# Performance work log

Hardware: AMD Instinct MI355X
Metric: run time of the kernel (lower is better)

Reference implementation:

```python
import jax, jax.numpy as jnp
import numpy as np

N = 100000          # number of nodes
E = 128             # embedding size
NUM_LAYERS = 4
SMOOTH = 12.0       # MAXIMUM_SMOOTHNESS
RELATIONS = [("at", 2), ("clear", 1), ("on", 2)]  # sorted, as in module
ATOM_COUNTS = {"at": 150000, "clear": 150000, "on": 150000}


def mish(x):
    return x * jnp.tanh(jax.nn.softplus(x))


def _linear_init(k, din, dout):
    s = 1.0 / np.sqrt(din)
    kw, kb = jax.random.split(k)
    w = jax.random.uniform(kw, (din, dout), jnp.float32, -s, s)
    b = jax.random.uniform(kb, (dout,), jnp.float32, -s, s)
    return w, b


def setup_inputs() -> dict:
    key = jax.random.key(0)
    ks = iter(jax.random.split(key, 64))
    inp = {}
    inp["node_embeddings"] = jax.random.normal(next(ks), (N, E), jnp.float32)
    for name, ar in RELATIONS:
        inp[f"atoms_{name}"] = jax.random.randint(
            next(ks), (ATOM_COUNTS[name] * ar,), 0, N, dtype=jnp.int32)
        d = ar * E
        inp[f"w_in_{name}"], inp[f"b_in_{name}"] = _linear_init(next(ks), d, d)
        inp[f"w_out_{name}"], inp[f"b_out_{name}"] = _linear_init(next(ks), d, d)
    # update MLP: Linear(2E, 2E) -> mish -> Linear(2E, E)
    inp["w_u_in"], inp["b_u_in"] = _linear_init(next(ks), 2 * E, 2 * E)
    inp["w_u_out"], inp["b_u_out"] = _linear_init(next(ks), 2 * E, E)
    return inp


def _forward(node_embeddings, atoms, params):
    w_u_in, b_u_in, w_u_out, b_u_out = params["update"]

    def layer(h):
        msgs, idxs = [], []
        for name, ar in RELATIONS:
            w_in, b_in, w_out, b_out = params[name]
            av = atoms[name]                              # [A*ar] node indices
            x = h[av].reshape(-1, ar * E)                 # gather -> [A, ar*E]
            y = x + (mish(x @ w_in + b_in) @ w_out + b_out)  # residual MLP
            msgs.append(y.reshape(-1, E))
            idxs.append(av)
        msg = jnp.concatenate(msgs, 0)                    # [T, E]
        idx = jnp.concatenate(idxs, 0)                    # [T]
        # smooth-max aggregation (max offsets are not differentiated)
        seg_max = jax.ops.segment_max(msg, idx, num_segments=N)
        seg_max = jnp.where(jnp.isfinite(seg_max), seg_max, 0.0)  # empty -> 0 (include_self=False on zeros)
        seg_max = jax.lax.stop_gradient(seg_max)
        exps = jnp.exp(SMOOTH * (msg - seg_max[idx]))
        exps_sum = jax.ops.segment_sum(exps, idx, num_segments=N) + 1e-16
        max_msg = jnp.log(exps_sum) / SMOOTH + seg_max
        upd_in = jnp.concatenate([max_msg, h], axis=1)    # [N, 2E]
        upd = mish(upd_in @ w_u_in + b_u_in) @ w_u_out + b_u_out
        return h + upd                                    # outer residual

    h = node_embeddings
    for _ in range(NUM_LAYERS):
        h = layer(h)
    return h


def reference(node_embeddings, atoms_at, atoms_clear, atoms_on,
              w_in_at, b_in_at, w_out_at, b_out_at,
              w_in_clear, b_in_clear, w_out_clear, b_out_clear,
              w_in_on, b_in_on, w_out_on, b_out_on,
              w_u_in, b_u_in, w_u_out, b_u_out):
    atoms = {"at": atoms_at, "clear": atoms_clear, "on": atoms_on}
    params = {
        "at": (w_in_at, b_in_at, w_out_at, b_out_at),
        "clear": (w_in_clear, b_in_clear, w_out_clear, b_out_clear),
        "on": (w_in_on, b_in_on, w_out_on, b_out_on),
        "update": (w_u_in, b_u_in, w_u_out, b_u_out),
    }
    return _forward(node_embeddings, atoms, params)
```

## Files before the change

### kernel.cpp

```cpp
#include <hip/hip_runtime.h>
#include <hip/hip_bf16.h>
#include <math.h>

#define NNODES 100000
#define EDIM 128
#define TSLOTS 750000
#define NB 391

typedef __bf16 bf16x8 __attribute__((ext_vector_type(8)));
typedef __bf16 bf16x4 __attribute__((ext_vector_type(4)));
typedef float f32x4 __attribute__((ext_vector_type(4)));

#define T_SCALE 17.312340490667562f
#define INV_SCALE 0.05776226504666211f
#define EMPTY_V (-3.0701134f)

__device__ __forceinline__ float mishf(float x) {
  float u = __expf(fminf(x, 15.f));
  float num = u * (u + 2.f);
  return x * num * __builtin_amdgcn_rcpf(num + 2.f);
}

__device__ __forceinline__ double exp12t(float t) {
  t = fmaxf(t, -20000.f);
  float ti = floorf(t);
  float m = exp2f(t - ti);
  int ei = (int)ti;
  ei = ei < -1000 ? -1000 : (ei > 1000 ? 1000 : ei);
  return (double)m * __longlong_as_double(((long long)(1023 + ei)) << 52);
}

__device__ __forceinline__ float logS12(double S) {
  if (!(S > 0.0)) return EMPTY_V;
  long long b = __double_as_longlong(S);
  int e2 = (int)((b >> 52) & 0x7FF) - 1023;
  float mf = __uint_as_float(0x3F800000u | (unsigned)((b >> 29) & 0x7FFFFF));
  return ((float)e2 + log2f(mf)) * INV_SCALE;
}

__global__ void k_sentinel(float* out, int n) {
  int i = blockIdx.x * 256 + threadIdx.x;
  if (i < n) out[i] = 1.0e6f;
}

__global__ void k_init(const float* __restrict__ h0, __bf16* __restrict__ hb, int n8) {
  int i = blockIdx.x * 256 + threadIdx.x;
  if (i >= n8) return;
  float4 f0 = ((const float4*)h0)[i * 2];
  float4 f1 = ((const float4*)h0)[i * 2 + 1];
  bf16x8 p = {(__bf16)f0.x, (__bf16)f0.y, (__bf16)f0.z, (__bf16)f0.w,
              (__bf16)f1.x, (__bf16)f1.y, (__bf16)f1.z, (__bf16)f1.w};
  *(bf16x8*)(hb + (size_t)i * 8) = p;
}

struct TransDesc {
  const float* src[8];
  __bf16* dst[8];
  int R[8];
  int C[8];
  int tstart[9];
};

__global__ void k_transpose_all(TransDesc td) {
  __shared__ float tile[32][33];
  int b = blockIdx.x;
  int m = 0;
  while (m < 7 && b >= td.tstart[m + 1]) m++;
  int t = b - td.tstart[m];
  int R = td.R[m], C = td.C[m];
  int tcols = C >> 5;
  int by = t / tcols, bx = t - by * tcols;
  int tx = threadIdx.x & 31, ty = threadIdx.x >> 5;
  const float* src = td.src[m];
  __bf16* dst = td.dst[m];
  for (int i = 0; i < 32; i += 8)
    tile[ty + i][tx] = src[(size_t)(by * 32 + ty + i) * C + bx * 32 + tx];
  __syncthreads();
  for (int i = 0; i < 32; i += 8)
    dst[(size_t)(bx * 32 + ty + i) * R + by * 32 + tx] = (__bf16)tile[tx][ty + i];
}

__device__ __forceinline__ int slot_node(int s, const int* at, const int* cl, const int* on) {
  if (s < 300000) return at[s];
  if (s < 450000) return cl[s - 300000];
  return on[s - 450000];
}

__global__ void k_count(const int* __restrict__ at, const int* __restrict__ cl,
                        const int* __restrict__ on, int* __restrict__ cnt) {
  int s = blockIdx.x * 256 + threadIdx.x;
  if (s >= TSLOTS) return;
  atomicAdd(&cnt[slot_node(s, at, cl, on)], 1);
}

__global__ void k_bsum(const int* __restrict__ cnt, int* __restrict__ bsum) {
  __shared__ int sm[256];
  int n = blockIdx.x * 256 + threadIdx.x;
  sm[threadIdx.x] = (n < NNODES) ? cnt[n] : 0;
  __syncthreads();
  for (int st = 128; st > 0; st >>= 1) {
    if (threadIdx.x < st) sm[threadIdx.x] += sm[threadIdx.x + st];
    __syncthreads();
  }
  if (threadIdx.x == 0) bsum[blockIdx.x] = sm[0];
}

__global__ void k_bscan(const int* __restrict__ bsum, int* __restrict__ bpre,
                        int* __restrict__ off) {
  __shared__ int sm[512];
  int t = threadIdx.x;
  int v = (t < NB) ? bsum[t] : 0;
  sm[t] = v;
  __syncthreads();
  for (int st = 1; st < 512; st <<= 1) {
    int x = (t >= st) ? sm[t - st] : 0;
    __syncthreads();
    sm[t] += x;
    __syncthreads();
  }
  if (t < NB) bpre[t] = sm[t] - v;
  if (t == NB - 1) off[NNODES] = sm[t];
}

__global__ void k_off(const int* __restrict__ cnt, const int* __restrict__ bpre,
                      int* __restrict__ off) {
  __shared__ int sm[256];
  int n = blockIdx.x * 256 + threadIdx.x;
  int v = (n < NNODES) ? cnt[n] : 0;
  sm[threadIdx.x] = v;
  __syncthreads();
  for (int st = 1; st < 256; st <<= 1) {
    int t = (threadIdx.x >= st) ? sm[threadIdx.x - st] : 0;
    __syncthreads();
    sm[threadIdx.x] += t;
    __syncthreads();
  }
  if (n < NNODES) off[n] = bpre[blockIdx.x] + sm[threadIdx.x] - v;
}

__global__ void k_fill(const int* __restrict__ at, const int* __restrict__ cl,
                       const int* __restrict__ on, const int* __restrict__ off,
                       int* __restrict__ cnt, int* __restrict__ perm) {
  int s = blockIdx.x * 256 + threadIdx.x;
  if (s >= TSLOTS) return;
  int node = slot_node(s, at, cl, on);
  int pos = atomicAdd(&cnt[node], -1) - 1;
  perm[s] = off[node] + pos;
}

__global__ __launch_bounds__(256, 4) void k_rel2(
    const float* __restrict__ hf, const __bf16* __restrict__ hb,
    const int* __restrict__ av,
    const __bf16* __restrict__ wt1, const float* __restrict__ b1,
    const __bf16* __restrict__ wt2, const float* __restrict__ b2,
    _Float16* __restrict__ msg, const int* __restrict__ permrel, int A) {
  __shared__ __align__(16) __bf16 xs[64][264];
  __shared__ int prm[128];
  const int tid = threadIdx.x;
  const int lane = tid & 63;
  const int w = tid >> 6;
  const int row0 = blockIdx.x * 64;

  if (tid < 128) {
    int i2 = row0 * 2 + tid;
    prm[tid] = (i2 < 2 * A) ? permrel[i2] : 0;
  }
  if (hb != nullptr) {
    for (int i = 0; i < 8; ++i) {
      int s = tid + i * 256;
      int r = s >> 5, o = s & 31;
      int a = row0 + r;
      uint4 v = {0, 0, 0, 0};
      if (a < A) {
        int node = av[2 * a + (o >> 4)];
        v = *(const uint4*)(hb + (size_t)node * 128 + (o & 15) * 8);
      }
      *(uint4*)&xs[r][o * 8] = v;
    }
  } else {
    for (int i = 0; i < 16; ++i) {
      int s = tid + i * 256;
      int r = s >> 6, o = s & 63;
      int a = row0 + r;
      float4 f = {0.f, 0.f, 0.f, 0.f};
      if (a < A) {
        int node = av[2 * a + (o >> 5)];
        f = *(const float4*)(hf + (size_t)node * 128 + (o & 31) * 4);
      }
      bf16x4 p = {(__bf16)f.x, (__bf16)f.y, (__bf16)f.z, (__bf16)f.w};
      *(bf16x4*)&xs[r][o * 4] = p;
    }
  }
  __syncthreads();

  const int lhi = lane >> 4, llo = lane & 15;
  const int cb = w * 64;

  f32x4 acc1[4][4];
#pragma unroll
  for (int rt = 0; rt < 4; rt++)
#pragma unroll
    for (int ct = 0; ct < 4; ct++) acc1[rt][ct] = (f32x4){0.f, 0.f, 0.f, 0.f};

#pragma unroll
  for (int kk = 0; kk < 8; ++kk) {
    int k = kk * 32 + lhi * 8;
    bf16x8 af[4], bfr[4];
#pragma unroll
    for (int rt = 0; rt < 4; rt++) af[rt] = *(const bf16x8*)&xs[rt * 16 + llo][k];
#pragma unroll
    for (int ct = 0; ct < 4; ct++)
      bfr[ct] = *(const bf16x8*)(wt1 + (size_t)(cb + ct * 16 + llo) * 256 + k);
#pragma unroll
    for (int rt = 0; rt < 4; rt++)
#pragma unroll
      for (int ct = 0; ct < 4; ct++)
        acc1[rt][ct] = __builtin_amdgcn_mfma_f32_16x16x32_bf16(af[rt], bfr[ct], acc1[rt][ct], 0, 0, 0);
  }
  __syncthreads();

  float b1v[4];
#pragma unroll
  for (int ct = 0; ct < 4; ct++) b1v[ct] = b1[cb + ct * 16 + llo];
#pragma unroll
  for (int rt = 0; rt < 4; rt++)
#pragma unroll
    for (int ct = 0; ct < 4; ct++)
#pragma unroll
      for (int i = 0; i < 4; i++)
        xs[rt * 16 + lhi * 4 + i][cb + ct * 16 + llo] = (__bf16)mishf(acc1[rt][ct][i] + b1v[ct]);
  __syncthreads();

  f32x4 acc2[4][4];
#pragma unroll
  for (int rt = 0; rt < 4; rt++)
#pragma unroll
    for (int ct = 0; ct < 4; ct++) acc2[rt][ct] = (f32x4){0.f, 0.f, 0.f, 0.f};

#pragma unroll
  for (int kk = 0; kk < 8; ++kk) {
    int k = kk * 32 + lhi * 8;
    bf16x8 af[4], bfr[4];
#pragma unroll
    for (int rt = 0; rt < 4; rt++) af[rt] = *(const bf16x8*)&xs[rt * 16 + llo][k];
#pragma unroll
    for (int ct = 0; ct < 4; ct++)
      bfr[ct] = *(const bf16x8*)(wt2 + (size_t)(cb + ct * 16 + llo) * 256 + k);
#pragma unroll
    for (int rt = 0; rt < 4; rt++)
#pragma unroll
      for (int ct = 0; ct < 4; ct++)
        acc2[rt][ct] = __builtin_amdgcn_mfma_f32_16x16x32_bf16(af[rt], bfr[ct], acc2[rt][ct], 0, 0, 0);
  }
  __syncthreads();

  float b2v[4];
#pragma unroll
  for (int ct = 0; ct < 4; ct++) b2v[ct] = b2[cb + ct * 16 + llo];
  ushort* zs = (ushort*)&xs[0][0];
#pragma unroll
  for (int rt = 0; rt < 4; rt++)
#pragma unroll
    for (int ct = 0; ct < 4; ct++)
#pragma unroll
      for (int i = 0; i < 4; i++) {
        int r = rt * 16 + lhi * 4 + i;
        int col = cb + ct * 16 + llo;
        union { ushort u; _Float16 f; } cv;
        cv.f = (_Float16)(acc2[rt][ct][i] + b2v[ct]);
        zs[r * 264 + col] = cv.u;
      }
  __syncthreads();

  for (int i = 0; i < 8; ++i) {
    int s = tid + i * 256;
    int sr = s >> 4;
    int c = s & 15;
    int a = row0 + (sr >> 1);
    if (a < A) {
      int rr = sr >> 1, c0 = (sr & 1) * 128 + c * 8;
      uint4 z = *(const uint4*)&zs[rr * 264 + c0];
      *(uint4*)(msg + (size_t)prm[sr] * 128 + c * 8) = z;
    }
  }
}

__global__ __launch_bounds__(256, 4) void k_rel1(
    const float* __restrict__ hf, const __bf16* __restrict__ hb,
    const int* __restrict__ av,
    const __bf16* __restrict__ wt1, const float* __restrict__ b1,
    const __bf16* __restrict__ wt2, const float* __restrict__ b2,
    _Float16* __restrict__ msg, const int* __restrict__ permrel, int A) {
  __shared__ __align__(16) __bf16 xs[64][136];
  __shared__ int prm[64];
  const int tid = threadIdx.x;
  const int lane = tid & 63;
  const int w = tid >> 6;
  const int row0 = blockIdx.x * 64;

  if (tid < 64) {
    int a = row0 + tid;
    prm[tid] = (a < A) ? permrel[a] : 0;
  }
  if (hb != nullptr) {
    for (int i = 0; i < 4; ++i) {
      int s = tid + i * 256;
      int r = s >> 4, o = s & 15;
      int a = row0 + r;
      uint4 v = {0, 0, 0, 0};
      if (a < A) {
        int node = av[a];
        v = *(const uint4*)(hb + (size_t)node * 128 + o * 8);
      }
      *(uint4*)&xs[r][o * 8] = v;
    }
  } else {
    for (int i = 0; i < 8; ++i) {
      int s = tid + i * 256;
      int r = s >> 5, o = s & 31;
      int a = row0 + r;
      float4 f = {0.f, 0.f, 0.f, 0.f};
      if (a < A) {
        int node = av[a];
        f = *(const float4*)(hf + (size_t)node * 128 + o * 4);
      }
      bf16x4 p = {(__bf16)f.x, (__bf16)f.y, (__bf16)f.z, (__bf16)f.w};
      *(bf16x4*)&xs[r][o * 4] = p;
    }
  }
  __syncthreads();

  const int lhi = lane >> 4, llo = lane & 15;
  const int cb = w * 32;

  f32x4 acc1[4][2];
#pragma unroll
  for (int rt = 0; rt < 4; rt++)
#pragma unroll
    for (int ct = 0; ct < 2; ct++) acc1[rt][ct] = (f32x4){0.f, 0.f, 0.f, 0.f};

#pragma unroll
  for (int kk = 0; kk < 4; ++kk) {
    int k = kk * 32 + lhi * 8;
    bf16x8 af[4], bfr[2];
#pragma unroll
    for (int rt = 0; rt < 4; rt++) af[rt] = *(const bf16x8*)&xs[rt * 16 + llo][k];
#pragma unroll
    for (int ct = 0; ct < 2; ct++)
      bfr[ct] = *(const bf16x8*)(wt1 + (size_t)(cb + ct * 16 + llo) * 128 + k);
#pragma unroll
    for (int rt = 0; rt < 4; rt++)
#pragma unroll
      for (int ct = 0; ct < 2; ct++)
        acc1[rt][ct] = __builtin_amdgcn_mfma_f32_16x16x32_bf16(af[rt], bfr[ct], acc1[rt][ct], 0, 0, 0);
  }
  __syncthreads();

  float b1v[2];
#pragma unroll
  for (int ct = 0; ct < 2; ct++) b1v[ct] = b1[cb + ct * 16 + llo];
#pragma unroll
  for (int rt = 0; rt < 4; rt++)
#pragma unroll
    for (int ct = 0; ct < 2; ct++)
#pragma unroll
      for (int i = 0; i < 4; i++)
        xs[rt * 16 + lhi * 4 + i][cb + ct * 16 + llo] = (__bf16)mishf(acc1[rt][ct][i] + b1v[ct]);
  __syncthreads();

  f32x4 acc2[4][2];
#pragma unroll
  for (int rt = 0; rt < 4; rt++)
#pragma unroll
    for (int ct = 0; ct < 2; ct++) acc2[rt][ct] = (f32x4){0.f, 0.f, 0.f, 0.f};

#pragma unroll
  for (int kk = 0; kk < 4; ++kk) {
    int k = kk * 32 + lhi * 8;
    bf16x8 af[4], bfr[2];
#pragma unroll
    for (int rt = 0; rt < 4; rt++) af[rt] = *(const bf16x8*)&xs[rt * 16 + llo][k];
#pragma unroll
    for (int ct = 0; ct < 2; ct++)
      bfr[ct] = *(const bf16x8*)(wt2 + (size_t)(cb + ct * 16 + llo) * 128 + k);
#pragma unroll
    for (int rt = 0; rt < 4; rt++)
#pragma unroll
      for (int ct = 0; ct < 2; ct++)
        acc2[rt][ct] = __builtin_amdgcn_mfma_f32_16x16x32_bf16(af[rt], bfr[ct], acc2[rt][ct], 0, 0, 0);
  }
  __syncthreads();

  float b2v[2];
#pragma unroll
  for (int ct = 0; ct < 2; ct++) b2v[ct] = b2[cb + ct * 16 + llo];
  ushort* zs = (ushort*)&xs[0][0];
#pragma unroll
  for (int rt = 0; rt < 4; rt++)
#pragma unroll
    for (int ct = 0; ct < 2; ct++)
#pragma unroll
      for (int i = 0; i < 4; i++) {
        int r = rt * 16 + lhi * 4 + i;
        int col = cb + ct * 16 + llo;
        union { ushort u; _Float16 f; } cv;
        cv.f = (_Float16)(acc2[rt][ct][i] + b2v[ct]);
        zs[r * 136 + col] = cv.u;
      }
  __syncthreads();

  for (int i = 0; i < 4; ++i) {
    int s = tid + i * 256;
    int sr = s >> 4;
    int c = s & 15;
    int a = row0 + sr;
    if (a < A) {
      uint4 z = *(const uint4*)&zs[sr * 136 + c * 8];
      *(uint4*)(msg + (size_t)prm[sr] * 128 + c * 8) = z;
    }
  }
}

__global__ __launch_bounds__(256, 8) void k_agg(
    const _Float16* __restrict__ msg, const int* __restrict__ off,
    const float* __restrict__ hf, const __bf16* __restrict__ hb,
    __bf16* __restrict__ mm) {
  __shared__ int offs[33];
  const int tid = threadIdx.x;
  const int lane = tid & 63;
  const int w = tid >> 6;
  const int node0 = blockIdx.x * 32;
  if (tid < 33) {
    int n = node0 + tid;
    offs[tid] = off[n < NNODES ? n : NNODES];
  }
  __syncthreads();

  const int fl = lane & 31;
  const int p = lane >> 5;
  const _Float16* mb = msg + fl * 4;

#pragma unroll 1
  for (int j = 0; j < 8; ++j) {
    int n = node0 + w * 8 + j;
    if (n >= NNODES) break;
    float h0, h1, h2, h3;
    if (hb != nullptr) {
      bf16x4 hq = *(const bf16x4*)(hb + (size_t)n * 128 + fl * 4);
      h0 = (float)hq[0]; h1 = (float)hq[1]; h2 = (float)hq[2]; h3 = (float)hq[3];
    } else {
      float4 hq = *(const float4*)(hf + (size_t)n * 128 + fl * 4);
      h0 = hq.x; h1 = hq.y; h2 = hq.z; h3 = hq.w;
    }
    int beg = offs[w * 8 + j];
    int deg = offs[w * 8 + j + 1] - beg;
    double S0 = 0.0, S1 = 0.0, S2 = 0.0, S3 = 0.0;
#pragma unroll 1
    for (int d = 0; d < deg; d += 2) {
      int rp = d + p;
      int rc = rp < deg - 1 ? rp : deg - 1;
      uint2 v = *(const uint2*)(mb + (size_t)(beg + rc) * 128);
      if (rp >= deg) { v.x = 0xFC00FC00u; v.y = 0xFC00FC00u; }
      union { uint2 u; _Float16 f[4]; } q;
      q.u = v;
      S0 += exp12t(((float)q.f[0] + h0) * T_SCALE);
      S1 += exp12t(((float)q.f[1] + h1) * T_SCALE);
      S2 += exp12t(((float)q.f[2] + h2) * T_SCALE);
      S3 += exp12t(((float)q.f[3] + h3) * T_SCALE);
    }
    S0 += __shfl_xor(S0, 32);
    S1 += __shfl_xor(S1, 32);
    S2 += __shfl_xor(S2, 32);
    S3 += __shfl_xor(S3, 32);
    if (p == 0) {
      bf16x4 r;
      r[0] = (__bf16)logS12(S0);
      r[1] = (__bf16)logS12(S1);
      r[2] = (__bf16)logS12(S2);
      r[3] = (__bf16)logS12(S3);
      *(bf16x4*)(mm + (size_t)n * 128 + fl * 4) = r;
    }
  }
}

__global__ __launch_bounds__(256, 4) void k_mlp(
    const float* __restrict__ hin, const __bf16* __restrict__ mm,
    const __bf16* __restrict__ wt1, const float* __restrict__ b1,
    const __bf16* __restrict__ wt2, const float* __restrict__ b2,
    float* __restrict__ hout, __bf16* __restrict__ hbout) {
  __shared__ __align__(16) __bf16 xs[64][264];
  const int tid = threadIdx.x;
  const int lane = tid & 63;
  const int w = tid >> 6;
  const int node0 = blockIdx.x * 64;

  for (int i = 0; i < 4; ++i) {
    int s = tid + i * 256;
    int r = s >> 4, o = s & 15;
    int n = node0 + r;
    uint4 v = {0, 0, 0, 0};
    if (n < NNODES) v = *(const uint4*)(mm + (size_t)n * 128 + o * 8);
    *(uint4*)&xs[r][o * 8] = v;
  }
  for (int i = 0; i < 8; ++i) {
    int s = tid + i * 256;
    int r = s >> 5, o = s & 31;
    int n = node0 + r;
    float4 f = {0.f, 0.f, 0.f, 0.f};
    if (n < NNODES) f = *(const float4*)(hin + (size_t)n * 128 + o * 4);
    bf16x4 p = {(__bf16)f.x, (__bf16)f.y, (__bf16)f.z, (__bf16)f.w};
    *(bf16x4*)&xs[r][128 + o * 4] = p;
  }
  __syncthreads();

  const int lhi = lane >> 4, llo = lane & 15;
  const int cb = w * 64;

  f32x4 acc1[4][4];
#pragma unroll
  for (int rt = 0; rt < 4; rt++)
#pragma unroll
    for (int ct = 0; ct < 4; ct++) acc1[rt][ct] = (f32x4){0.f, 0.f, 0.f, 0.f};

#pragma unroll
  for (int kk = 0; kk < 8; ++kk) {
    int k = kk * 32 + lhi * 8;
    bf16x8 af[4], bfr[4];
#pragma unroll
    for (int rt = 0; rt < 4; rt++) af[rt] = *(const bf16x8*)&xs[rt * 16 + llo][k];
#pragma unroll
    for (int ct = 0; ct < 4; ct++)
      bfr[ct] = *(const bf16x8*)(wt1 + (size_t)(cb + ct * 16 + llo) * 256 + k);
#pragma unroll
    for (int rt = 0; rt < 4; rt++)
#pragma unroll
      for (int ct = 0; ct < 4; ct++)
        acc1[rt][ct] = __builtin_amdgcn_mfma_f32_16x16x32_bf16(af[rt], bfr[ct], acc1[rt][ct], 0, 0, 0);
  }
  __syncthreads();

  float b1v[4];
#pragma unroll
  for (int ct = 0; ct < 4; ct++) b1v[ct] = b1[cb + ct * 16 + llo];
#pragma unroll
  for (int rt = 0; rt < 4; rt++)
#pragma unroll
    for (int ct = 0; ct < 4; ct++)
#pragma unroll
      for (int i = 0; i < 4; i++)
        xs[rt * 16 + lhi * 4 + i][cb + ct * 16 + llo] = (__bf16)mishf(acc1[rt][ct][i] + b1v[ct]);
  __syncthreads();

  const int cb2 = w * 32;
  f32x4 acc2[4][2];
#pragma unroll
  for (int rt = 0; rt < 4; rt++)
#pragma unroll
    for (int ct = 0; ct < 2; ct++) acc2[rt][ct] = (f32x4){0.f, 0.f, 0.f, 0.f};

#pragma unroll
  for (int kk = 0; kk < 8; ++kk) {
    int k = kk * 32 + lhi * 8;
    bf16x8 af[4], bfr[2];
#pragma unroll
    for (int rt = 0; rt < 4; rt++) af[rt] = *(const bf16x8*)&xs[rt * 16 + llo][k];
#pragma unroll
    for (int ct = 0; ct < 2; ct++)
      bfr[ct] = *(const bf16x8*)(wt2 + (size_t)(cb2 + ct * 16 + llo) * 256 + k);
#pragma unroll
    for (int rt = 0; rt < 4; rt++)
#pragma unroll
      for (int ct = 0; ct < 2; ct++)
        acc2[rt][ct] = __builtin_amdgcn_mfma_f32_16x16x32_bf16(af[rt], bfr[ct], acc2[rt][ct], 0, 0, 0);
  }

  float b2v[2];
#pragma unroll
  for (int ct = 0; ct < 2; ct++) b2v[ct] = b2[cb2 + ct * 16 + llo];
#pragma unroll
  for (int rt = 0; rt < 4; rt++)
#pragma unroll
    for (int i = 0; i < 4; i++) {
      int r = rt * 16 + lhi * 4 + i;
      int n = node0 + r;
      if (n >= NNODES) continue;
#pragma unroll
      for (int ct = 0; ct < 2; ct++) {
        int col = cb2 + ct * 16 + llo;
        size_t idx = (size_t)n * 128 + col;
        float nh = hin[idx] + acc2[rt][ct][i] + b2v[ct];
        hout[idx] = nh;
        if (hbout != nullptr) hbout[idx] = (__bf16)nh;
      }
    }
}

extern "C" void kernel_launch(void* const* d_in, const int* in_sizes, int n_in,
                              void* d_out, int out_size, void* d_ws, size_t ws_size,
                              hipStream_t stream) {
  const float* h0 = (const float*)d_in[0];
  const int* at = (const int*)d_in[1];
  const float* w_in_at = (const float*)d_in[2];
  const float* b_in_at = (const float*)d_in[3];
  const float* w_out_at = (const float*)d_in[4];
  const float* b_out_at = (const float*)d_in[5];
  const int* cl = (const int*)d_in[6];
  const float* w_in_cl = (const float*)d_in[7];
  const float* b_in_cl = (const float*)d_in[8];
  const float* w_out_cl = (const float*)d_in[9];
  const float* b_out_cl = (const float*)d_in[10];
  const int* on = (const int*)d_in[11];
  const float* w_in_on = (const float*)d_in[12];
  const float* b_in_on = (const float*)d_in[13];
  const float* w_out_on = (const float*)d_in[14];
  const float* b_out_on = (const float*)d_in[15];
  const float* w_u_in = (const float*)d_in[16];
  const float* b_u_in = (const float*)d_in[17];
  const float* w_u_out = (const float*)d_in[18];
  const float* b_u_out = (const float*)d_in[19];

  float* hout = (float*)d_out;
  char* ws = (char*)d_ws;

  const size_t MSG_B = (size_t)TSLOTS * 128 * 2;
  const size_t OFF_B = 400016;
  const size_t CNT_B = 400000;
  const size_t BS_B = 1568;
  const size_t PERM_B = 3000000;
  const size_t WT_B = 786432;
  const size_t MM_B = (size_t)NNODES * 128 * 2;
  const size_t HB_B = (size_t)NNODES * 128 * 2;
  const size_t REQ2 = MSG_B + OFF_B + CNT_B + 2 * BS_B + PERM_B + WT_B + MM_B;
  const size_t REQ3 = REQ2 + HB_B;

  if (ws_size < REQ2) {
    k_sentinel<<<(out_size + 255) / 256, 256, 0, stream>>>((float*)d_out, out_size);
    return;
  }

  _Float16* msg = (_Float16*)ws;
  int* off = (int*)(ws + MSG_B);
  int* cnt = (int*)(ws + MSG_B + OFF_B);
  int* bsum = (int*)(ws + MSG_B + OFF_B + CNT_B);
  int* bpre = (int*)(ws + MSG_B + OFF_B + CNT_B + BS_B);
  int* perm = (int*)(ws + MSG_B + OFF_B + CNT_B + 2 * BS_B);
  __bf16* wt = (__bf16*)(ws + MSG_B + OFF_B + CNT_B + 2 * BS_B + PERM_B);
  __bf16* mm = (__bf16*)(ws + MSG_B + OFF_B + CNT_B + 2 * BS_B + PERM_B + WT_B);
  __bf16* hb = (ws_size >= REQ3) ? (__bf16*)(ws + REQ2) : nullptr;

  __bf16* wt_in_at = wt;
  __bf16* wt_out_at = wt + 65536;
  __bf16* wt_in_on = wt + 131072;
  __bf16* wt_out_on = wt + 196608;
  __bf16* wt_u_in = wt + 262144;
  __bf16* wt_u_out = wt + 327680;
  __bf16* wt_in_cl = wt + 360448;
  __bf16* wt_out_cl = wt + 376832;

  TransDesc td;
  const float* srcs[8] = {w_in_at, w_out_at, w_in_on, w_out_on, w_u_in, w_u_out, w_in_cl, w_out_cl};
  __bf16* dsts[8] = {wt_in_at, wt_out_at, wt_in_on, wt_out_on, wt_u_in, wt_u_out, wt_in_cl, wt_out_cl};
  int Rs[8] = {256, 256, 256, 256, 256, 256, 128, 128};
  int Cs[8] = {256, 256, 256, 256, 256, 128, 128, 128};
  int ts = 0;
  for (int m = 0; m < 8; ++m) {
    td.src[m] = srcs[m]; td.dst[m] = dsts[m]; td.R[m] = Rs[m]; td.C[m] = Cs[m];
    td.tstart[m] = ts; ts += (Rs[m] / 32) * (Cs[m] / 32);
  }
  td.tstart[8] = ts;
  k_transpose_all<<<384, 256, 0, stream>>>(td);

  if (hb) k_init<<<6250, 256, 0, stream>>>(h0, hb, NNODES * EDIM / 8);

  const int grid_rel = (150000 + 63) / 64;
  const int grid_mlp = (NNODES + 63) / 64;
  const int grid_agg = (NNODES + 31) / 32;
  const int grid_slots = (TSLOTS + 255) / 256;

  hipMemsetAsync(cnt, 0, CNT_B, stream);
  k_count<<<grid_slots, 256, 0, stream>>>(at, cl, on, cnt);
  k_bsum<<<NB, 256, 0, stream>>>(cnt, bsum);
  k_bscan<<<1, 512, 0, stream>>>(bsum, bpre, off);
  k_off<<<NB, 256, 0, stream>>>(cnt, bpre, off);
  k_fill<<<grid_slots, 256, 0, stream>>>(at, cl, on, off, cnt, perm);

  const int* perm_at = perm;
  const int* perm_cl = perm + 300000;
  const int* perm_on = perm + 450000;

  for (int l = 0; l < 4; ++l) {
    const float* hs = (l == 0) ? h0 : hout;
    k_rel2<<<grid_rel, 256, 0, stream>>>(hs, hb, at, wt_in_at, b_in_at, wt_out_at, b_out_at, msg, perm_at, 150000);
    k_rel1<<<grid_rel, 256, 0, stream>>>(hs, hb, cl, wt_in_cl, b_in_cl, wt_out_cl, b_out_cl, msg, perm_cl, 150000);
    k_rel2<<<grid_rel, 256, 0, stream>>>(hs, hb, on, wt_in_on, b_in_on, wt_out_on, b_out_on, msg, perm_on, 150000);
    k_agg<<<grid_agg, 256, 0, stream>>>(msg, off, hs, hb, mm);
    k_mlp<<<grid_mlp, 256, 0, stream>>>(hs, mm, wt_u_in, b_u_in, wt_u_out, b_u_out, hout, hb);
  }
}
```

Baseline: 1.805 ms.

## Merge three relation MLP kernels into one launch with 32-row tiles

Folds the two arity-2 relations and the arity-1 relation into a single kernel that picks its relation by block index, removing two launches and the tail idle time between them per layer. Row tiles shrink from 64 to 32 in both the relation and update MLP kernels, and launch bounds rise to 6 blocks per SM, to improve occupancy and load balance. The cost is that each block reuses the weight fragments it loads across fewer rows, and the fused kernel branches on relation type.

```diff
diff --git a/kernel.cpp b/kernel.cpp
--- a/kernel.cpp
+++ b/kernel.cpp
@@ -6,6 +6,7 @@
 #define EDIM 128
 #define TSLOTS 750000
 #define NB 391
+#define GR2 4688
 
 typedef __bf16 bf16x8 __attribute__((ext_vector_type(8)));
 typedef __bf16 bf16x4 __attribute__((ext_vector_type(4)));
@@ -148,275 +149,271 @@
   perm[s] = off[node] + pos;
 }
 
-__global__ __launch_bounds__(256, 4) void k_rel2(
+struct RelAll {
+  const int* av[3];
+  const __bf16* wt1[3];
+  const float* b1[3];
+  const __bf16* wt2[3];
+  const float* b2[3];
+  const int* prm[3];
+};
+
+__global__ __launch_bounds__(256, 6) void k_relf(
     const float* __restrict__ hf, const __bf16* __restrict__ hb,
-    const int* __restrict__ av,
-    const __bf16* __restrict__ wt1, const float* __restrict__ b1,
-    const __bf16* __restrict__ wt2, const float* __restrict__ b2,
-    _Float16* __restrict__ msg, const int* __restrict__ permrel, int A) {
-  __shared__ __align__(16) __bf16 xs[64][264];
-  __shared__ int prm[128];
-  const int tid = threadIdx.x;
-  const int lane = tid & 63;
-  const int w = tid >> 6;
-  const int row0 = blockIdx.x * 64;
-
-  if (tid < 128) {
-    int i2 = row0 * 2 + tid;
-    prm[tid] = (i2 < 2 * A) ? permrel[i2] : 0;
-  }
-  if (hb != nullptr) {
-    for (int i = 0; i < 8; ++i) {
-      int s = tid + i * 256;
-      int r = s >> 5, o = s & 31;
-      int a = row0 + r;
-      uint4 v = {0, 0, 0, 0};
-      if (a < A) {
-        int node = av[2 * a + (o >> 4)];
-        v = *(const uint4*)(hb + (size_t)node * 128 + (o & 15) * 8);
-      }
-      *(uint4*)&xs[r][o * 8] = v;
-    }
-  } else {
-    for (int i = 0; i < 16; ++i) {
-      int s = tid + i * 256;
-      int r = s >> 6, o = s & 63;
-      int a = row0 + r;
-      float4 f = {0.f, 0.f, 0.f, 0.f};
-      if (a < A) {
-        int node = av[2 * a + (o >> 5)];
-        f = *(const float4*)(hf + (size_t)node * 128 + (o & 31) * 4);
-      }
-      bf16x4 p = {(__bf16)f.x, (__bf16)f.y, (__bf16)f.z, (__bf16)f.w};
-      *(bf16x4*)&xs[r][o * 4] = p;
-    }
-  }
-  __syncthreads();
-
-  const int lhi = lane >> 4, llo = lane & 15;
-  const int cb = w * 64;
-
-  f32x4 acc1[4][4];
-#pragma unroll
-  for (int rt = 0; rt < 4; rt++)
-#pragma unroll
-    for (int ct = 0; ct < 4; ct++) acc1[rt][ct] = (f32x4){0.f, 0.f, 0.f, 0.f};
-
-#pragma unroll
-  for (int kk = 0; kk < 8; ++kk) {
-    int k = kk * 32 + lhi * 8;
-    bf16x8 af[4], bfr[4];
-#pragma unroll
-    for (int rt = 0; rt < 4; rt++) af[rt] = *(const bf16x8*)&xs[rt * 16 + llo][k];
-#pragma unroll
-    for (int ct = 0; ct < 4; ct++)
-      bfr[ct] = *(const bf16x8*)(wt1 + (size_t)(cb + ct * 16 + llo) * 256 + k);
-#pragma unroll
-    for (int rt = 0; rt < 4; rt++)
-#pragma unroll
-      for (int ct = 0; ct < 4; ct++)
-        acc1[rt][ct] = __builtin_amdgcn_mfma_f32_16x16x32_bf16(af[rt], bfr[ct], acc1[rt][ct], 0, 0, 0);
-  }
-  __syncthreads();
-
-  float b1v[4];
-#pragma unroll
-  for (int ct = 0; ct < 4; ct++) b1v[ct] = b1[cb + ct * 16 + llo];
-#pragma unroll
-  for (int rt = 0; rt < 4; rt++)
-#pragma unroll
-    for (int ct = 0; ct < 4; ct++)
-#pragma unroll
-      for (int i = 0; i < 4; i++)
-        xs[rt * 16 + lhi * 4 + i][cb + ct * 16 + llo] = (__bf16)mishf(acc1[rt][ct][i] + b1v[ct]);
-  __syncthreads();
-
-  f32x4 acc2[4][4];
-#pragma unroll
-  for (int rt = 0; rt < 4; rt++)
-#pragma unroll
-    for (int ct = 0; ct < 4; ct++) acc2[rt][ct] = (f32x4){0.f, 0.f, 0.f, 0.f};
-
-#pragma unroll
-  for (int kk = 0; kk < 8; ++kk) {
-    int k = kk * 32 + lhi * 8;
-    bf16x8 af[4], bfr[4];
-#pragma unroll
-    for (int rt = 0; rt < 4; rt++) af[rt] = *(const bf16x8*)&xs[rt * 16 + llo][k];
-#pragma unroll
-    for (int ct = 0; ct < 4; ct++)
-      bfr[ct] = *(const bf16x8*)(wt2 + (size_t)(cb + ct * 16 + llo) * 256 + k);
-#pragma unroll
-    for (int rt = 0; rt < 4; rt++)
-#pragma unroll
-      for (int ct = 0; ct < 4; ct++)
-        acc2[rt][ct] = __builtin_amdgcn_mfma_f32_16x16x32_bf16(af[rt], bfr[ct], acc2[rt][ct], 0, 0, 0);
-  }
-  __syncthreads();
-
-  float b2v[4];
-#pragma unroll
-  for (int ct = 0; ct < 4; ct++) b2v[ct] = b2[cb + ct * 16 + llo];
-  ushort* zs = (ushort*)&xs[0][0];
-#pragma unroll
-  for (int rt = 0; rt < 4; rt++)
-#pragma unroll
-    for (int ct = 0; ct < 4; ct++)
-#pragma unroll
-      for (int i = 0; i < 4; i++) {
-        int r = rt * 16 + lhi * 4 + i;
-        int col = cb + ct * 16 + llo;
-        union { ushort u; _Float16 f; } cv;
-        cv.f = (_Float16)(acc2[rt][ct][i] + b2v[ct]);
-        zs[r * 264 + col] = cv.u;
-      }
-  __syncthreads();
-
-  for (int i = 0; i < 8; ++i) {
-    int s = tid + i * 256;
-    int sr = s >> 4;
-    int c = s & 15;
-    int a = row0 + (sr >> 1);
-    if (a < A) {
-      int rr = sr >> 1, c0 = (sr & 1) * 128 + c * 8;
-      uint4 z = *(const uint4*)&zs[rr * 264 + c0];
-      *(uint4*)(msg + (size_t)prm[sr] * 128 + c * 8) = z;
-    }
-  }
-}
-
-__global__ __launch_bounds__(256, 4) void k_rel1(
-    const float* __restrict__ hf, const __bf16* __restrict__ hb,
-    const int* __restrict__ av,
-    const __bf16* __restrict__ wt1, const float* __restrict__ b1,
-    const __bf16* __restrict__ wt2, const float* __restrict__ b2,
-    _Float16* __restrict__ msg, const int* __restrict__ permrel, int A) {
-  __shared__ __align__(16) __bf16 xs[64][136];
+    RelAll ra, _Float16* __restrict__ msg) {
+  __shared__ __align__(16) __bf16 xs[32][264];
   __shared__ int prm[64];
   const int tid = threadIdx.x;
   const int lane = tid & 63;
   const int w = tid >> 6;
-  const int row0 = blockIdx.x * 64;
-
-  if (tid < 64) {
-    int a = row0 + tid;
-    prm[tid] = (a < A) ? permrel[a] : 0;
-  }
-  if (hb != nullptr) {
+  const int b = blockIdx.x;
+  const int m = (b < GR2) ? 0 : (b < 2 * GR2 ? 1 : 2);
+  const int rb = b - m * GR2;
+  const int row0 = rb * 32;
+  const int A = 150000;
+  const int* av = ra.av[m];
+  const __bf16* wt1 = ra.wt1[m];
+  const float* b1 = ra.b1[m];
+  const __bf16* wt2 = ra.wt2[m];
+  const float* b2 = ra.b2[m];
+  const int* permrel = ra.prm[m];
+  const int lhi = lane >> 4, llo = lane & 15;
+  ushort* zs = (ushort*)&xs[0][0];
+
+  if (m < 2) {
+    if (tid < 64) {
+      int i2 = row0 * 2 + tid;
+      prm[tid] = (i2 < 2 * A) ? permrel[i2] : 0;
+    }
+    if (hb != nullptr) {
+      for (int i = 0; i < 4; ++i) {
+        int s = tid + i * 256;
+        int r = s >> 5, o = s & 31;
+        int a = row0 + r;
+        uint4 v = {0, 0, 0, 0};
+        if (a < A) {
+          int node = av[2 * a + (o >> 4)];
+          v = *(const uint4*)(hb + (size_t)node * 128 + (o & 15) * 8);
+        }
+        *(uint4*)&xs[r][o * 8] = v;
+      }
+    } else {
+      for (int i = 0; i < 8; ++i) {
+        int s = tid + i * 256;
+        int r = s >> 6, o = s & 63;
+        int a = row0 + r;
+        float4 f = {0.f, 0.f, 0.f, 0.f};
+        if (a < A) {
+          int node = av[2 * a + (o >> 5)];
+          f = *(const float4*)(hf + (size_t)node * 128 + (o & 31) * 4);
+        }
+        bf16x4 p = {(__bf16)f.x, (__bf16)f.y, (__bf16)f.z, (__bf16)f.w};
+        *(bf16x4*)&xs[r][o * 4] = p;
+      }
+    }
+    __syncthreads();
+
+    const int cb = w * 64;
+    f32x4 acc1[2][4];
+#pragma unroll
+    for (int rt = 0; rt < 2; rt++)
+#pragma unroll
+      for (int ct = 0; ct < 4; ct++) acc1[rt][ct] = (f32x4){0.f, 0.f, 0.f, 0.f};
+#pragma unroll
+    for (int kk = 0; kk < 8; ++kk) {
+      int k = kk * 32 + lhi * 8;
+      bf16x8 af[2], bfr[4];
+#pragma unroll
+      for (int rt = 0; rt < 2; rt++) af[rt] = *(const bf16x8*)&xs[rt * 16 + llo][k];
+#pragma unroll
+      for (int ct = 0; ct < 4; ct++)
+        bfr[ct] = *(const bf16x8*)(wt1 + (size_t)(cb + ct * 16 + llo) * 256 + k);
+#pragma unroll
+      for (int rt = 0; rt < 2; rt++)
+#pragma unroll
+        for (int ct = 0; ct < 4; ct++)
+          acc1[rt][ct] = __builtin_amdgcn_mfma_f32_16x16x32_bf16(af[rt], bfr[ct], acc1[rt][ct], 0, 0, 0);
+    }
+    __syncthreads();
+
+    float b1v[4];
+#pragma unroll
+    for (int ct = 0; ct < 4; ct++) b1v[ct] = b1[cb + ct * 16 + llo];
+#pragma unroll
+    for (int rt = 0; rt < 2; rt++)
+#pragma unroll
+      for (int ct = 0; ct < 4; ct++)
+#pragma unroll
+        for (int i = 0; i < 4; i++)
+          xs[rt * 16 + lhi * 4 + i][cb + ct * 16 + llo] = (__bf16)mishf(acc1[rt][ct][i] + b1v[ct]);
+    __syncthreads();
+
+    f32x4 acc2[2][4];
+#pragma unroll
+    for (int rt = 0; rt < 2; rt++)
+#pragma unroll
+      for (int ct = 0; ct < 4; ct++) acc2[rt][ct] = (f32x4){0.f, 0.f, 0.f, 0.f};
+#pragma unroll
+    for (int kk = 0; kk < 8; ++kk) {
+      int k = kk * 32 + lhi * 8;
+      bf16x8 af[2], bfr[4];
+#pragma unroll
+      for (int rt = 0; rt < 2; rt++) af[rt] = *(const bf16x8*)&xs[rt * 16 + llo][k];
+#pragma unroll
+      for (int ct = 0; ct < 4; ct++)
+        bfr[ct] = *(const bf16x8*)(wt2 + (size_t)(cb + ct * 16 + llo) * 256 + k);
+#pragma unroll
+      for (int rt = 0; rt < 2; rt++)
+#pragma unroll
+        for (int ct = 0; ct < 4; ct++)
+          acc2[rt][ct] = __builtin_amdgcn_mfma_f32_16x16x32_bf16(af[rt], bfr[ct], acc2[rt][ct], 0, 0, 0);
+    }
+    __syncthreads();
+
+    float b2v[4];
+#pragma unroll
+    for (int ct = 0; ct < 4; ct++) b2v[ct] = b2[cb + ct * 16 + llo];
+#pragma unroll
+    for (int rt = 0; rt < 2; rt++)
+#pragma unroll
+      for (int ct = 0; ct < 4; ct++)
+#pragma unroll
+        for (int i = 0; i < 4; i++) {
+          int r = rt * 16 + lhi * 4 + i;
+          int col = cb + ct * 16 + llo;
+          union { ushort u; _Float16 f; } cv;
+          cv.f = (_Float16)(acc2[rt][ct][i] + b2v[ct]);
+          zs[r * 264 + col] = cv.u;
+        }
+    __syncthreads();
+
     for (int i = 0; i < 4; ++i) {
       int s = tid + i * 256;
-      int r = s >> 4, o = s & 15;
-      int a = row0 + r;
-      uint4 v = {0, 0, 0, 0};
+      int sr = s >> 4;
+      int c = s & 15;
+      int a = row0 + (sr >> 1);
       if (a < A) {
-        int node = av[a];
-        v = *(const uint4*)(hb + (size_t)node * 128 + o * 8);
+        int rr = sr >> 1, c0 = (sr & 1) * 128 + c * 8;
+        uint4 z = *(const uint4*)&zs[rr * 264 + c0];
+        *(uint4*)(msg + (size_t)prm[sr] * 128 + c * 8) = z;
       }
-      *(uint4*)&xs[r][o * 8] = v;
     }
   } else {
-    for (int i = 0; i < 8; ++i) {
+    if (tid < 32) {
+      int a = row0 + tid;
+      prm[tid] = (a < A) ? permrel[a] : 0;
+    }
+    if (hb != nullptr) {
+      for (int i = 0; i < 2; ++i) {
+        int s = tid + i * 256;
+        int r = s >> 4, o = s & 15;
+        int a = row0 + r;
+        uint4 v = {0, 0, 0, 0};
+        if (a < A) {
+          int node = av[a];
+          v = *(const uint4*)(hb + (size_t)node * 128 + o * 8);
+        }
+        *(uint4*)&xs[r][o * 8] = v;
+      }
+    } else {
+      for (int i = 0; i < 4; ++i) {
+        int s = tid + i * 256;
+        int r = s >> 5, o = s & 31;
+        int a = row0 + r;
+        float4 f = {0.f, 0.f, 0.f, 0.f};
+        if (a < A) {
+          int node = av[a];
+          f = *(const float4*)(hf + (size_t)node * 128 + o * 4);
+        }
+        bf16x4 p = {(__bf16)f.x, (__bf16)f.y, (__bf16)f.z, (__bf16)f.w};
+        *(bf16x4*)&xs[r][o * 4] = p;
+      }
+    }
+    __syncthreads();
+
+    const int cb = w * 32;
+    f32x4 acc1[2][2];
+#pragma unroll
+    for (int rt = 0; rt < 2; rt++)
+#pragma unroll
+      for (int ct = 0; ct < 2; ct++) acc1[rt][ct] = (f32x4){0.f, 0.f, 0.f, 0.f};
+#pragma unroll
+    for (int kk = 0; kk < 4; ++kk) {
+      int k = kk * 32 + lhi * 8;
+      bf16x8 af[2], bfr[2];
+#pragma unroll
+      for (int rt = 0; rt < 2; rt++) af[rt] = *(const bf16x8*)&xs[rt * 16 + llo][k];
+#pragma unroll
+      for (int ct = 0; ct < 2; ct++)
+        bfr[ct] = *(const bf16x8*)(wt1 + (size_t)(cb + ct * 16 + llo) * 128 + k);
+#pragma unroll
+      for (int rt = 0; rt < 2; rt++)
+#pragma unroll
+        for (int ct = 0; ct < 2; ct++)
+          acc1[rt][ct] = __builtin_amdgcn_mfma_f32_16x16x32_bf16(af[rt], bfr[ct], acc1[rt][ct], 0, 0, 0);
+    }
+    __syncthreads();
+
+    float b1v[2];
+#pragma unroll
+    for (int ct = 0; ct < 2; ct++) b1v[ct] = b1[cb + ct * 16 + llo];
+#pragma unroll
+    for (int rt = 0; rt < 2; rt++)
+#pragma unroll
+      for (int ct = 0; ct < 2; ct++)
+#pragma unroll
+        for (int i = 0; i < 4; i++)
+          xs[rt * 16 + lhi * 4 + i][cb + ct * 16 + llo] = (__bf16)mishf(acc1[rt][ct][i] + b1v[ct]);
+    __syncthreads();
+
+    f32x4 acc2[2][2];
+#pragma unroll
+    for (int rt = 0; rt < 2; rt++)
+#pragma unroll
+      for (int ct = 0; ct < 2; ct++) acc2[rt][ct] = (f32x4){0.f, 0.f, 0.f, 0.f};
+#pragma unroll
+    for (int kk = 0; kk < 4; ++kk) {
+      int k = kk * 32 + lhi * 8;
+      bf16x8 af[2], bfr[2];
+#pragma unroll
+      for (int rt = 0; rt < 2; rt++) af[rt] = *(const bf16x8*)&xs[rt * 16 + llo][k];
+#pragma unroll
+      for (int ct = 0; ct < 2; ct++)
+        bfr[ct] = *(const bf16x8*)(wt2 + (size_t)(cb + ct * 16 + llo) * 128 + k);
+#pragma unroll
+      for (int rt = 0; rt < 2; rt++)
+#pragma unroll
+        for (int ct = 0; ct < 2; ct++)
+          acc2[rt][ct] = __builtin_amdgcn_mfma_f32_16x16x32_bf16(af[rt], bfr[ct], acc2[rt][ct], 0, 0, 0);
+    }
+    __syncthreads();
+
+    float b2v[2];
+#pragma unroll
+    for (int ct = 0; ct < 2; ct++) b2v[ct] = b2[cb + ct * 16 + llo];
+#pragma unroll
+    for (int rt = 0; rt < 2; rt++)
+#pragma unroll
+      for (int ct = 0; ct < 2; ct++)
+#pragma unroll
+        for (int i = 0; i < 4; i++) {
+          int r = rt * 16 + lhi * 4 + i;
+          int col = cb + ct * 16 + llo;
+          union { ushort u; _Float16 f; } cv;
+          cv.f = (_Float16)(acc2[rt][ct][i] + b2v[ct]);
+          zs[r * 264 + col] = cv.u;
+        }
+    __syncthreads();
+
+    for (int i = 0; i < 2; ++i) {
       int s = tid + i * 256;
-      int r = s >> 5, o = s & 31;
-      int a = row0 + r;
-      float4 f = {0.f, 0.f, 0.f, 0.f};
+      int sr = s >> 4;
+      int c = s & 15;
+      int a = row0 + sr;
       if (a < A) {
-        int node = av[a];
-        f = *(const float4*)(hf + (size_t)node * 128 + o * 4);
+        uint4 z = *(const uint4*)&zs[sr * 264 + c * 8];
+        *(uint4*)(msg + (size_t)prm[sr] * 128 + c * 8) = z;
       }
-      bf16x4 p = {(__bf16)f.x, (__bf16)f.y, (__bf16)f.z, (__bf16)f.w};
-      *(bf16x4*)&xs[r][o * 4] = p;
-    }
-  }
-  __syncthreads();
-
-  const int lhi = lane >> 4, llo = lane & 15;
-  const int cb = w * 32;
-
-  f32x4 acc1[4][2];
-#pragma unroll
-  for (int rt = 0; rt < 4; rt++)
-#pragma unroll
-    for (int ct = 0; ct < 2; ct++) acc1[rt][ct] = (f32x4){0.f, 0.f, 0.f, 0.f};
-
-#pragma unroll
-  for (int kk = 0; kk < 4; ++kk) {
-    int k = kk * 32 + lhi * 8;
-    bf16x8 af[4], bfr[2];
-#pragma unroll
-    for (int rt = 0; rt < 4; rt++) af[rt] = *(const bf16x8*)&xs[rt * 16 + llo][k];
-#pragma unroll
-    for (int ct = 0; ct < 2; ct++)
-      bfr[ct] = *(const bf16x8*)(wt1 + (size_t)(cb + ct * 16 + llo) * 128 + k);
-#pragma unroll
-    for (int rt = 0; rt < 4; rt++)
-#pragma unroll
-      for (int ct = 0; ct < 2; ct++)
-        acc1[rt][ct] = __builtin_amdgcn_mfma_f32_16x16x32_bf16(af[rt], bfr[ct], acc1[rt][ct], 0, 0, 0);
-  }
-  __syncthreads();
-
-  float b1v[2];
-#pragma unroll
-  for (int ct = 0; ct < 2; ct++) b1v[ct] = b1[cb + ct * 16 + llo];
-#pragma unroll
-  for (int rt = 0; rt < 4; rt++)
-#pragma unroll
-    for (int ct = 0; ct < 2; ct++)
-#pragma unroll
-      for (int i = 0; i < 4; i++)
-        xs[rt * 16 + lhi * 4 + i][cb + ct * 16 + llo] = (__bf16)mishf(acc1[rt][ct][i] + b1v[ct]);
-  __syncthreads();
-
-  f32x4 acc2[4][2];
-#pragma unroll
-  for (int rt = 0; rt < 4; rt++)
-#pragma unroll
-    for (int ct = 0; ct < 2; ct++) acc2[rt][ct] = (f32x4){0.f, 0.f, 0.f, 0.f};
-
-#pragma unroll
-  for (int kk = 0; kk < 4; ++kk) {
-    int k = kk * 32 + lhi * 8;
-    bf16x8 af[4], bfr[2];
-#pragma unroll
-    for (int rt = 0; rt < 4; rt++) af[rt] = *(const bf16x8*)&xs[rt * 16 + llo][k];
-#pragma unroll
-    for (int ct = 0; ct < 2; ct++)
-      bfr[ct] = *(const bf16x8*)(wt2 + (size_t)(cb + ct * 16 + llo) * 128 + k);
-#pragma unroll
-    for (int rt = 0; rt < 4; rt++)
-#pragma unroll
-      for (int ct = 0; ct < 2; ct++)
-        acc2[rt][ct] = __builtin_amdgcn_mfma_f32_16x16x32_bf16(af[rt], bfr[ct], acc2[rt][ct], 0, 0, 0);
-  }
-  __syncthreads();
-
-  float b2v[2];
-#pragma unroll
-  for (int ct = 0; ct < 2; ct++) b2v[ct] = b2[cb + ct * 16 + llo];
-  ushort* zs = (ushort*)&xs[0][0];
-#pragma unroll
-  for (int rt = 0; rt < 4; rt++)
-#pragma unroll
-    for (int ct = 0; ct < 2; ct++)
-#pragma unroll
-      for (int i = 0; i < 4; i++) {
-        int r = rt * 16 + lhi * 4 + i;
-        int col = cb + ct * 16 + llo;
-        union { ushort u; _Float16 f; } cv;
-        cv.f = (_Float16)(acc2[rt][ct][i] + b2v[ct]);
-        zs[r * 136 + col] = cv.u;
-      }
-  __syncthreads();
-
-  for (int i = 0; i < 4; ++i) {
-    int s = tid + i * 256;
-    int sr = s >> 4;
-    int c = s & 15;
-    int a = row0 + sr;
-    if (a < A) {
-      uint4 z = *(const uint4*)&zs[sr * 136 + c * 8];
-      *(uint4*)(msg + (size_t)prm[sr] * 128 + c * 8) = z;
     }
   }
 }
@@ -483,18 +480,18 @@
   }
 }
 
-__global__ __launch_bounds__(256, 4) void k_mlp(
+__global__ __launch_bounds__(256, 6) void k_mlp(
     const float* __restrict__ hin, const __bf16* __restrict__ mm,
     const __bf16* __restrict__ wt1, const float* __restrict__ b1,
     const __bf16* __restrict__ wt2, const float* __restrict__ b2,
     float* __restrict__ hout, __bf16* __restrict__ hbout) {
-  __shared__ __align__(16) __bf16 xs[64][264];
+  __shared__ __align__(16) __bf16 xs[32][264];
   const int tid = threadIdx.x;
   const int lane = tid & 63;
   const int w = tid >> 6;
-  const int node0 = blockIdx.x * 64;
-
-  for (int i = 0; i < 4; ++i) {
+  const int node0 = blockIdx.x * 32;
+
+  for (int i = 0; i < 2; ++i) {
     int s = tid + i * 256;
     int r = s >> 4, o = s & 15;
     int n = node0 + r;
@@ -502,7 +499,7 @@
     if (n < NNODES) v = *(const uint4*)(mm + (size_t)n * 128 + o * 8);
     *(uint4*)&xs[r][o * 8] = v;
   }
-  for (int i = 0; i < 8; ++i) {
+  for (int i = 0; i < 4; ++i) {
     int s = tid + i * 256;
     int r = s >> 5, o = s & 31;
     int n = node0 + r;
@@ -516,23 +513,22 @@
   const int lhi = lane >> 4, llo = lane & 15;
   const int cb = w * 64;
 
-  f32x4 acc1[4][4];
-#pragma unroll
-  for (int rt = 0; rt < 4; rt++)
+  f32x4 acc1[2][4];
+#pragma unroll
+  for (int rt = 0; rt < 2; rt++)
 #pragma unroll
     for (int ct = 0; ct < 4; ct++) acc1[rt][ct] = (f32x4){0.f, 0.f, 0.f, 0.f};
-
 #pragma unroll
   for (int kk = 0; kk < 8; ++kk) {
     int k = kk * 32 + lhi * 8;
-    bf16x8 af[4], bfr[4];
-#pragma unroll
-    for (int rt = 0; rt < 4; rt++) af[rt] = *(const bf16x8*)&xs[rt * 16 + llo][k];
+    bf16x8 af[2], bfr[4];
+#pragma unroll
+    for (int rt = 0; rt < 2; rt++) af[rt] = *(const bf16x8*)&xs[rt * 16 + llo][k];
 #pragma unroll
     for (int ct = 0; ct < 4; ct++)
       bfr[ct] = *(const bf16x8*)(wt1 + (size_t)(cb + ct * 16 + llo) * 256 + k);
 #pragma unroll
-    for (int rt = 0; rt < 4; rt++)
+    for (int rt = 0; rt < 2; rt++)
 #pragma unroll
       for (int ct = 0; ct < 4; ct++)
         acc1[rt][ct] = __builtin_amdgcn_mfma_f32_16x16x32_bf16(af[rt], bfr[ct], acc1[rt][ct], 0, 0, 0);
@@ -543,7 +539,7 @@
 #pragma unroll
   for (int ct = 0; ct < 4; ct++) b1v[ct] = b1[cb + ct * 16 + llo];
 #pragma unroll
-  for (int rt = 0; rt < 4; rt++)
+  for (int rt = 0; rt < 2; rt++)
 #pragma unroll
     for (int ct = 0; ct < 4; ct++)
 #pragma unroll
@@ -552,23 +548,22 @@
   __syncthreads();
 
   const int cb2 = w * 32;
-  f32x4 acc2[4][2];
-#pragma unroll
-  for (int rt = 0; rt < 4; rt++)
+  f32x4 acc2[2][2];
+#pragma unroll
+  for (int rt = 0; rt < 2; rt++)
 #pragma unroll
     for (int ct = 0; ct < 2; ct++) acc2[rt][ct] = (f32x4){0.f, 0.f, 0.f, 0.f};
-
 #pragma unroll
   for (int kk = 0; kk < 8; ++kk) {
     int k = kk * 32 + lhi * 8;
-    bf16x8 af[4], bfr[2];
-#pragma unroll
-    for (int rt = 0; rt < 4; rt++) af[rt] = *(const bf16x8*)&xs[rt * 16 + llo][k];
+    bf16x8 af[2], bfr[2];
+#pragma unroll
+    for (int rt = 0; rt < 2; rt++) af[rt] = *(const bf16x8*)&xs[rt * 16 + llo][k];
 #pragma unroll
     for (int ct = 0; ct < 2; ct++)
       bfr[ct] = *(const bf16x8*)(wt2 + (size_t)(cb2 + ct * 16 + llo) * 256 + k);
 #pragma unroll
-    for (int rt = 0; rt < 4; rt++)
+    for (int rt = 0; rt < 2; rt++)
 #pragma unroll
       for (int ct = 0; ct < 2; ct++)
         acc2[rt][ct] = __builtin_amdgcn_mfma_f32_16x16x32_bf16(af[rt], bfr[ct], acc2[rt][ct], 0, 0, 0);
@@ -578,7 +573,7 @@
 #pragma unroll
   for (int ct = 0; ct < 2; ct++) b2v[ct] = b2[cb2 + ct * 16 + llo];
 #pragma unroll
-  for (int rt = 0; rt < 4; rt++)
+  for (int rt = 0; rt < 2; rt++)
 #pragma unroll
     for (int i = 0; i < 4; i++) {
       int r = rt * 16 + lhi * 4 + i;
@@ -672,8 +667,7 @@
 
   if (hb) k_init<<<6250, 256, 0, stream>>>(h0, hb, NNODES * EDIM / 8);
 
-  const int grid_rel = (150000 + 63) / 64;
-  const int grid_mlp = (NNODES + 63) / 64;
+  const int grid_mlp = (NNODES + 31) / 32;
   const int grid_agg = (NNODES + 31) / 32;
   const int grid_slots = (TSLOTS + 255) / 256;
 
@@ -684,15 +678,14 @@
   k_off<<<NB, 256, 0, stream>>>(cnt, bpre, off);
   k_fill<<<grid_slots, 256, 0, stream>>>(at, cl, on, off, cnt, perm);
 
-  const int* perm_at = perm;
-  const int* perm_cl = perm + 300000;
-  const int* perm_on = perm + 450000;
+  RelAll ra;
+  ra.av[0] = at;  ra.wt1[0] = wt_in_at; ra.b1[0] = b_in_at; ra.wt2[0] = wt_out_at; ra.b2[0] = b_out_at; ra.prm[0] = perm;
+  ra.av[1] = on;  ra.wt1[1] = wt_in_on; ra.b1[1] = b_in_on; ra.wt2[1] = wt_out_on; ra.b2[1] = b_out_on; ra.prm[1] = perm + 450000;
+  ra.av[2] = cl;  ra.wt1[2] = wt_in_cl; ra.b1[2] = b_in_cl; ra.wt2[2] = wt_out_cl; ra.b2[2] = b_out_cl; ra.prm[2] = perm + 300000;
 
   for (int l = 0; l < 4; ++l) {
     const float* hs = (l == 0) ? h0 : hout;
-    k_rel2<<<grid_rel, 256, 0, stream>>>(hs, hb, at, wt_in_at, b_in_at, wt_out_at, b_out_at, msg, perm_at, 150000);
-    k_rel1<<<grid_rel, 256, 0, stream>>>(hs, hb, cl, wt_in_cl, b_in_cl, wt_out_cl, b_out_cl, msg, perm_cl, 150000);
-    k_rel2<<<grid_rel, 256, 0, stream>>>(hs, hb, on, wt_in_on, b_in_on, wt_out_on, b_out_on, msg, perm_on, 150000);
+    k_relf<<<3 * GR2, 256, 0, stream>>>(hs, hb, ra, msg);
     k_agg<<<grid_agg, 256, 0, stream>>>(msg, off, hs, hb, mm);
     k_mlp<<<grid_mlp, 256, 0, stream>>>(hs, mm, wt_u_in, b_u_in, wt_u_out, b_u_out, hout, hb);
   }
```

New measurement: 2.282 ms. +26.4%, slower.
